# Kernel tuning notes

Measured on AMD Instinct MI355X. Metric: run time of the kernel, lower is better.

Reference implementation:

```python
import jax, jax.numpy as jnp
import numpy as np

D_MODEL = 1024
N_HEADS = 16
HEAD_DIM = D_MODEL // N_HEADS  # 64
WINDOW = 15
NUM_RANDOM = 2
B, L = 2, 2048


def setup_inputs() -> dict:
    key = jax.random.key(0)
    ks = jax.random.split(key, 5)
    x = jax.random.normal(ks[0], (B, L, D_MODEL), dtype=jnp.float32)
    # rotary angles: theta[t, j] = t / 10000^(2j/head_dim), shape [1, L, head_dim//2]
    inv_freq = 1.0 / (10000.0 ** (jnp.arange(0, HEAD_DIM, 2, dtype=jnp.float32) / HEAD_DIM))
    t = jnp.arange(L, dtype=jnp.float32)
    freqs = (t[:, None] * inv_freq[None, :])[None].astype(jnp.float32)  # [1,L,32]
    scale = 0.02
    wq = jax.random.normal(ks[1], (D_MODEL, D_MODEL), dtype=jnp.float32) * scale
    wk = jax.random.normal(ks[2], (D_MODEL, D_MODEL), dtype=jnp.float32) * scale
    wv = jax.random.normal(ks[3], (D_MODEL, D_MODEL), dtype=jnp.float32) * scale
    wo = jax.random.normal(ks[4], (D_MODEL, D_MODEL), dtype=jnp.float32) * scale
    return {"x": x, "freqs": freqs, "wq": wq, "wk": wk, "wv": wv, "wo": wo}


def _rope(t, cos, sin):
    # t: [B,H,L,hd]; interpret last dim as (hd/2, 2) complex pairs and rotate.
    tr = t.reshape(*t.shape[:-1], -1, 2)
    re, im = tr[..., 0], tr[..., 1]
    out_re = re * cos - im * sin
    out_im = re * sin + im * cos
    return jnp.stack([out_re, out_im], axis=-1).reshape(t.shape)


def _bigbird_mask(Lq):
    ii = jnp.arange(Lq)[:, None]
    jj = jnp.arange(Lq)[None, :]
    causal = jj <= ii
    window = jnp.abs(ii - jj) <= (WINDOW // 2)
    glob = (ii == 0) | (jj == 0)
    # random mask: per row i, NUM_RANDOM indices uniform in [0, i]
    rkey = jax.random.key(42)
    u = jax.random.uniform(rkey, (Lq, NUM_RANDOM))
    ridx = jnp.floor(u * (jnp.arange(Lq, dtype=jnp.float32)[:, None] + 1.0)).astype(jnp.int32)
    rmask = jnp.zeros((Lq, Lq), dtype=bool).at[jnp.arange(Lq)[:, None], ridx].set(True)
    # rows with <= NUM_RANDOM causal options attend to all of them
    rmask = rmask | (causal & (ii < NUM_RANDOM))
    return (causal & (window | rmask)) | glob  # [L,L]


def reference(x, freqs, wq, wk, wv, wo):
    b, l, _ = x.shape
    q = (x @ wq.T).reshape(b, l, N_HEADS, HEAD_DIM).transpose(0, 2, 1, 3)  # [B,H,L,hd]
    k = (x @ wk.T).reshape(b, l, N_HEADS, HEAD_DIM).transpose(0, 2, 1, 3)
    v = (x @ wv.T).reshape(b, l, N_HEADS, HEAD_DIM).transpose(0, 2, 1, 3)
    cos = jnp.cos(freqs[:, :l])[:, None]  # [1,1,L,hd/2]
    sin = jnp.sin(freqs[:, :l])[:, None]
    q = _rope(q, cos, sin)
    k = _rope(k, cos, sin)
    attn_mask = _bigbird_mask(l)  # [L,L], broadcast over B,H
    scale = 1.0 / jnp.sqrt(jnp.float32(HEAD_DIM))
    scores = jnp.einsum("bhqd,bhkd->bhqk", q, k) * scale
    scores = jnp.where(attn_mask[None, None], scores, jnp.finfo(scores.dtype).min)
    p = jax.nn.softmax(scores, axis=-1)
    out = jnp.einsum("bhqk,bhkd->bhqd", p, v)
    out = out.transpose(0, 2, 1, 3).reshape(b, l, D_MODEL)
    return out @ wo.T
```

## Files before the change

kernel.cpp:

```cpp
#include <hip/hip_runtime.h>
#include <math.h>

#define SEQ_L 2048
#define DM 1024
#define NH 16
#define HD 64
#define NB 2
#define KD 1024
#define ND 1024

typedef __bf16 bf16;
typedef __bf16 bf16x8 __attribute__((ext_vector_type(8)));
typedef __bf16 bf16x4 __attribute__((ext_vector_type(4)));
typedef __bf16 bf16x2 __attribute__((ext_vector_type(2)));
typedef float f32x4 __attribute__((ext_vector_type(4)));

__device__ inline uint32_t rotl32(uint32_t v, int n) { return (v << n) | (v >> (32 - n)); }

__device__ inline void threefry(uint32_t x0, uint32_t x1, uint32_t* o0, uint32_t* o1) {
  const uint32_t ks0 = 0u, ks1 = 42u, ks2 = 0u ^ 42u ^ 0x1BD11BDAu;
  x0 += ks0; x1 += ks1;
#define TF_R(rr) { x0 += x1; x1 = rotl32(x1, rr); x1 ^= x0; }
  TF_R(13) TF_R(15) TF_R(26) TF_R(6)
  x0 += ks1; x1 += ks2 + 1u;
  TF_R(17) TF_R(29) TF_R(16) TF_R(24)
  x0 += ks2; x1 += ks0 + 2u;
  TF_R(13) TF_R(15) TF_R(26) TF_R(6)
  x0 += ks0; x1 += ks1 + 3u;
  TF_R(17) TF_R(29) TF_R(16) TF_R(24)
  x0 += ks1; x1 += ks2 + 4u;
  TF_R(13) TF_R(15) TF_R(26) TF_R(6)
  x0 += ks2; x1 += ks0 + 5u;
#undef TF_R
  *o0 = x0; *o1 = x1;
}

__device__ inline int rand_col(int i, int s) {
  uint32_t o0, o1;
  threefry(0u, (uint32_t)(2 * i + s), &o0, &o1);
  uint32_t bits = o0 ^ o1;
  float u = __uint_as_float((bits >> 9) | 0x3f800000u) - 1.0f;
  return (int)floorf(u * (float)(i + 1));
}

__global__ void prep_kernel(const float* __restrict__ x,
                            const float* __restrict__ w0, const float* __restrict__ w1,
                            const float* __restrict__ w2, const float* __restrict__ w3,
                            const float* __restrict__ freqs,
                            bf16* __restrict__ xb,
                            bf16* __restrict__ o0, bf16* __restrict__ o1,
                            bf16* __restrict__ o2, bf16* __restrict__ o3,
                            int* __restrict__ ctab, float2* __restrict__ rtab) {
  const int bx = blockIdx.x;
  const int t = threadIdx.x;
  if (bx < 8192) {
    const float* src;
    bf16* dst;
    int idx;
    if (bx < 4096) { src = x; dst = xb; idx = bx * 256 + t; }
    else {
      int widx = bx - 4096;
      int wsel = widx >> 10;
      switch (wsel) {
        case 0: src = w0; dst = o0; break;
        case 1: src = w1; dst = o1; break;
        case 2: src = w2; dst = o2; break;
        default: src = w3; dst = o3; break;
      }
      idx = (widx & 1023) * 256 + t;
    }
    float4 vv = ((const float4*)src)[idx];
    bf16x4 ov;
    ov[0] = (bf16)vv.x; ov[1] = (bf16)vv.y; ov[2] = (bf16)vv.z; ov[3] = (bf16)vv.w;
    *(bf16x4*)(dst + (size_t)idx * 4) = ov;
    return;
  }
  if (bx < 8200) {
    const int i = (bx - 8192) * 256 + t;
    int cols[11]; int nc = 0;
    if (i >= 1) {
      int lo = i - 7; if (lo < 0) lo = 0;
      for (int j = lo; j <= i; ++j) cols[nc++] = j;
      if (lo > 0) cols[nc++] = 0;
#pragma unroll
      for (int s = 0; s < 2; ++s) {
        int rj = rand_col(i, s);
        bool dup = false;
        for (int c2 = 0; c2 < nc; ++c2) dup |= (cols[c2] == rj);
        if (!dup) cols[nc++] = rj;
      }
    }
    for (int c2 = nc; c2 < 11; ++c2) cols[c2] = -1;
#pragma unroll
    for (int c2 = 0; c2 < 11; ++c2) ctab[i * 12 + c2] = cols[c2];
    ctab[i * 12 + 11] = nc;
    return;
  }
  const int idx = (bx - 8200) * 256 + t;
  float s, c;
  sincosf(freqs[idx], &s, &c);
  rtab[idx] = make_float2(c, s);
}

__device__ inline void gld16(const bf16* g, bf16* l) {
  __builtin_amdgcn_global_load_lds((const __attribute__((address_space(1))) void*)g,
                                   (__attribute__((address_space(3))) void*)l, 16, 0, 0);
}

__global__ __launch_bounds__(256, 4) void qkv_gemm_kernel(
    const bf16* __restrict__ xb, const bf16* __restrict__ wqb, const bf16* __restrict__ wkb,
    const bf16* __restrict__ wvb, bf16* __restrict__ qb, bf16* __restrict__ kb, bf16* __restrict__ vb,
    const float2* __restrict__ rtab) {
  __shared__ __align__(16) bf16 As[64 * 64];
  __shared__ __align__(16) bf16 Bs[3][64 * 64];
  const bf16* Ws[3] = {wqb, wkb, wvb};
  bf16* Ds[3] = {qb, kb, vb};

  const int t = threadIdx.x;
  const int lane = t & 63;
  const int w = t >> 6;
  const int wm = (w >> 1) * 32;
  const int wn = (w & 1) * 32;
  const int m0 = blockIdx.x * 64;
  const int n0 = blockIdx.y * 64;
  const int l15 = lane & 15;
  const int kq = lane >> 4;

  f32x4 acc[3][2][2] = {};

  for (int k0 = 0; k0 < KD; k0 += 64) {
#pragma unroll
    for (int n = 0; n < 2; ++n) {
      const int s = n * 256 + t;
      const int row = s >> 3;
      const int ch = (s & 7) ^ (row & 7);
      gld16(xb + (size_t)(m0 + row) * KD + k0 + ch * 8, As + s * 8);
    }
#pragma unroll
    for (int j = 0; j < 3; ++j)
#pragma unroll
      for (int n = 0; n < 2; ++n) {
        const int s = n * 256 + t;
        const int row = s >> 3;
        const int ch = (s & 7) ^ (row & 7);
        gld16(Ws[j] + (size_t)(n0 + row) * KD + k0 + ch * 8, &Bs[j][s * 8]);
      }
    __syncthreads();
#pragma unroll
    for (int ks = 0; ks < 2; ++ks) {
      const int cb = ks * 4 + kq;
      bf16x8 af[2];
#pragma unroll
      for (int mt = 0; mt < 2; ++mt) {
        const int row = wm + mt * 16 + l15;
        af[mt] = *(const bf16x8*)(As + row * 64 + ((cb ^ (row & 7)) * 8));
      }
#pragma unroll
      for (int j = 0; j < 3; ++j) {
        bf16x8 bfr[2];
#pragma unroll
        for (int nt = 0; nt < 2; ++nt) {
          const int row = wn + nt * 16 + l15;
          bfr[nt] = *(const bf16x8*)(&Bs[j][row * 64 + ((cb ^ (row & 7)) * 8)]);
        }
#pragma unroll
        for (int mt = 0; mt < 2; ++mt)
#pragma unroll
          for (int nt = 0; nt < 2; ++nt)
            acc[j][mt][nt] = __builtin_amdgcn_mfma_f32_16x16x32_bf16(af[mt], bfr[nt], acc[j][mt][nt], 0, 0, 0);
      }
    }
    __syncthreads();
  }
  const int colb = n0 + wn + l15;
  const int rowb = m0 + wm + (lane >> 4) * 4;
  const int odd = l15 & 1;
#pragma unroll
  for (int j = 0; j < 3; ++j) {
    bf16* D = Ds[j];
    const bool dorope = (j < 2);
#pragma unroll
    for (int mt = 0; mt < 2; ++mt)
#pragma unroll
      for (int nt = 0; nt < 2; ++nt) {
        const int col = colb + nt * 16;
        const int jj = (col & 63) >> 1;
#pragma unroll
        for (int rr = 0; rr < 4; ++rr) {
          float val = acc[j][mt][nt][rr];
          float other = __shfl_xor(val, 1);
          if (!odd) {
            const int row = rowb + mt * 16 + rr;
            float lo, hi;
            if (dorope) {
              float2 cs = rtab[(row & (SEQ_L - 1)) * 32 + jj];
              lo = val * cs.x - other * cs.y;
              hi = val * cs.y + other * cs.x;
            } else { lo = val; hi = other; }
            bf16x2 p; p[0] = (bf16)lo; p[1] = (bf16)hi;
            *(bf16x2*)(D + (size_t)row * ND + col) = p;
          }
        }
      }
  }
}

__global__ __launch_bounds__(256, 2) void out_gemm_kernel(
    bf16* __restrict__ ab, const bf16* __restrict__ wob, float* __restrict__ out,
    const float* __restrict__ pm, const float* __restrict__ pz, const float* __restrict__ pv) {
  const int t = threadIdx.x;
  const int m0 = blockIdx.x * 64;
  const int n0 = blockIdx.y * 128;

  if (blockIdx.x == 0 || blockIdx.x == 32) {
    const int b = blockIdx.x == 0 ? 0 : 1;
#pragma unroll
    for (int e = t; e < DM; e += 256) {
      const int h = e >> 6, d = e & 63;
      const int base = b * 128 + h * 8;
      float M = -1e30f;
#pragma unroll
      for (int c = 0; c < 8; ++c) M = fmaxf(M, pm[base + c]);
      float Z = 0.f, od = 0.f;
#pragma unroll
      for (int c = 0; c < 8; ++c) {
        float sc = __expf(pm[base + c] - M);
        Z += pz[base + c] * sc;
        od += pv[(base + c) * 64 + d] * sc;
      }
      ab[(size_t)b * SEQ_L * DM + e] = (bf16)(od / Z);
    }
    __syncthreads();
  }

  __shared__ __align__(16) bf16 As[64 * 64];
  __shared__ __align__(16) bf16 Bs[128 * 64];
  const int lane = t & 63;
  const int wave = t >> 6;
  const int wm = (wave >> 1) * 32;
  const int wn = (wave & 1) * 64;
  const int l15 = lane & 15;
  const int kq = lane >> 4;

  f32x4 acc[2][4] = {};

  for (int k0 = 0; k0 < KD; k0 += 64) {
#pragma unroll
    for (int n = 0; n < 2; ++n) {
      const int s = n * 256 + t;
      const int row = s >> 3;
      const int ch = (s & 7) ^ (row & 7);
      gld16(ab + (size_t)(m0 + row) * KD + k0 + ch * 8, As + s * 8);
    }
#pragma unroll
    for (int n = 0; n < 4; ++n) {
      const int s = n * 256 + t;
      const int row = s >> 3;
      const int ch = (s & 7) ^ (row & 7);
      gld16(wob + (size_t)(n0 + row) * KD + k0 + ch * 8, Bs + s * 8);
    }
    __syncthreads();
#pragma unroll
    for (int ks = 0; ks < 2; ++ks) {
      const int cb = ks * 4 + kq;
      bf16x8 af[2], bfr[4];
#pragma unroll
      for (int mt = 0; mt < 2; ++mt) {
        const int row = wm + mt * 16 + l15;
        af[mt] = *(const bf16x8*)(As + row * 64 + ((cb ^ (row & 7)) * 8));
      }
#pragma unroll
      for (int nt = 0; nt < 4; ++nt) {
        const int row = wn + nt * 16 + l15;
        bfr[nt] = *(const bf16x8*)(Bs + row * 64 + ((cb ^ (row & 7)) * 8));
      }
#pragma unroll
      for (int mt = 0; mt < 2; ++mt)
#pragma unroll
        for (int nt = 0; nt < 4; ++nt)
          acc[mt][nt] = __builtin_amdgcn_mfma_f32_16x16x32_bf16(af[mt], bfr[nt], acc[mt][nt], 0, 0, 0);
    }
    __syncthreads();
  }
  const int colb = n0 + wn + l15;
  const int rowb = m0 + wm + (lane >> 4) * 4;
#pragma unroll
  for (int mt = 0; mt < 2; ++mt)
#pragma unroll
    for (int nt = 0; nt < 4; ++nt)
#pragma unroll
      for (int rr = 0; rr < 4; ++rr)
        out[(size_t)(rowb + mt * 16 + rr) * ND + colb + nt * 16] = acc[mt][nt][rr];
}

__global__ __launch_bounds__(256, 2) void attn_kernel(const bf16* __restrict__ q, const bf16* __restrict__ k,
                                                      const bf16* __restrict__ v, bf16* __restrict__ o,
                                                      const int* __restrict__ ctab,
                                                      float* __restrict__ pm, float* __restrict__ pz,
                                                      float* __restrict__ pv) {
  const int t = threadIdx.x;
  const int lane = t & 63;
  const int w = t >> 6;

  __shared__ float sbuf[256];
  __shared__ float redm[4], redz[4];
  __shared__ float part[4][64];

  if (blockIdx.x >= 256) {
    const int sbx = blockIdx.x - 256;
    const int b = sbx >> 9;
    const int tt = sbx & 511;
    const int tile = ((tt & 7) << 6) + (tt >> 3);
    const int i = tile * 4 + 1 + w;
    if (i >= SEQ_L) return;
    const size_t bb = (size_t)b * SEQ_L * DM;
    const int eo = lane * 16;

    const bf16* qrow = q + bb + (size_t)i * DM + eo;
    bf16x8 qv0 = *(const bf16x8*)(qrow);
    bf16x8 qv1 = *(const bf16x8*)(qrow + 8);

    const int4* cp = (const int4*)(ctab + i * 12);
    int4 ca = cp[0], cb = cp[1], cc = cp[2];
    int cols[11] = {ca.x, ca.y, ca.z, ca.w, cb.x, cb.y, cb.z, cb.w, cc.x, cc.y, cc.z};

    bf16x8 kv[11][2], vv[11][2];
#pragma unroll
    for (int c = 0; c < 11; ++c) {
      int cj = cols[c] < 0 ? 0 : cols[c];
      const bf16* krow = k + bb + (size_t)cj * DM + eo;
      kv[c][0] = *(const bf16x8*)(krow);
      kv[c][1] = *(const bf16x8*)(krow + 8);
    }
#pragma unroll
    for (int c = 0; c < 11; ++c) {
      int cj = cols[c] < 0 ? 0 : cols[c];
      const bf16* vrow = v + bb + (size_t)cj * DM + eo;
      vv[c][0] = *(const bf16x8*)(vrow);
      vv[c][1] = *(const bf16x8*)(vrow + 8);
    }

    float sv[11];
#pragma unroll
    for (int c = 0; c < 11; ++c) {
      float acc = 0.f;
#pragma unroll
      for (int e = 0; e < 8; ++e)
        acc += (float)qv0[e] * (float)kv[c][0][e] + (float)qv1[e] * (float)kv[c][1][e];
      sv[c] = acc;
    }
#pragma unroll
    for (int c = 0; c < 11; ++c) {
      sv[c] += __shfl_xor(sv[c], 1);
      sv[c] += __shfl_xor(sv[c], 2);
      sv[c] = cols[c] < 0 ? -1e30f : sv[c] * 0.125f;
    }
    float m = -1e30f;
#pragma unroll
    for (int c = 0; c < 11; ++c) m = fmaxf(m, sv[c]);
    float z = 0.f;
#pragma unroll
    for (int c = 0; c < 11; ++c) { sv[c] = __expf(sv[c] - m); z += sv[c]; }
    const float inv = 1.f / z;

    float oa[16] = {};
#pragma unroll
    for (int c = 0; c < 11; ++c) {
#pragma unroll
      for (int e = 0; e < 8; ++e) {
        oa[e]     += sv[c] * (float)vv[c][0][e];
        oa[8 + e] += sv[c] * (float)vv[c][1][e];
      }
    }
    bf16x8 ov0, ov1;
#pragma unroll
    for (int e = 0; e < 8; ++e) {
      ov0[e] = (bf16)(oa[e] * inv);
      ov1[e] = (bf16)(oa[8 + e] * inv);
    }
    bf16* orow = o + bb + (size_t)i * DM + eo;
    *(bf16x8*)(orow) = ov0;
    *(bf16x8*)(orow + 8) = ov1;
    return;
  }

  const int idx = blockIdx.x;
  const int b = idx >> 7;
  const int rem = idx & 127;
  const int h = rem >> 3;
  const int c = rem & 7;
  const size_t hb = (size_t)b * SEQ_L * DM + (size_t)h * HD;
  const int j = c * 256 + t;

  bf16x8 qv8[8];
#pragma unroll
  for (int cc = 0; cc < 8; ++cc) qv8[cc] = *(const bf16x8*)(q + hb + cc * 8);

  float acc = 0.f;
#pragma unroll
  for (int cc = 0; cc < 8; ++cc) {
    bf16x8 kv = *(const bf16x8*)(k + hb + (size_t)j * DM + cc * 8);
#pragma unroll
    for (int e = 0; e < 8; ++e) acc += (float)qv8[cc][e] * (float)kv[e];
  }
  float s = acc * 0.125f;
  float mloc = s;
#pragma unroll
  for (int off = 32; off > 0; off >>= 1) mloc = fmaxf(mloc, __shfl_xor(mloc, off));
  if (lane == 0) redm[w] = mloc;
  __syncthreads();
  const float m = fmaxf(fmaxf(redm[0], redm[1]), fmaxf(redm[2], redm[3]));

  float e = __expf(s - m);
  sbuf[t] = e;
  float zloc = e;
#pragma unroll
  for (int off = 32; off > 0; off >>= 1) zloc += __shfl_xor(zloc, off);
  if (lane == 0) redz[w] = zloc;
  __syncthreads();
  const float zc = redz[0] + redz[1] + redz[2] + redz[3];

  float oa = 0.f;
  for (int jj = w; jj < 256; jj += 4)
    oa += sbuf[jj] * (float)v[hb + (size_t)(c * 256 + jj) * DM + lane];
  part[w][lane] = oa;
  __syncthreads();
  if (t < 64) pv[idx * 64 + t] = part[0][t] + part[1][t] + part[2][t] + part[3][t];
  if (t == 0) { pm[idx] = m; pz[idx] = zc; }
}

extern "C" void kernel_launch(void* const* d_in, const int* in_sizes, int n_in,
                              void* d_out, int out_size, void* d_ws, size_t ws_size,
                              hipStream_t stream) {
  const float* x     = (const float*)d_in[0];
  const float* freqs = (const float*)d_in[1];
  const float* wq    = (const float*)d_in[2];
  const float* wk    = (const float*)d_in[3];
  const float* wv    = (const float*)d_in[4];
  const float* wo    = (const float*)d_in[5];
  float* out = (float*)d_out;

  char* ws = (char*)d_ws;
  bf16* xb  = (bf16*)(ws + 0);
  bf16* wqb = (bf16*)(ws + 8388608);
  bf16* wkb = (bf16*)(ws + 10485760);
  bf16* wvb = (bf16*)(ws + 12582912);
  bf16* wob = (bf16*)(ws + 14680064);
  bf16* qb  = (bf16*)(ws + 16777216);
  bf16* kb  = (bf16*)(ws + 25165824);
  bf16* vb  = (bf16*)(ws + 33554432);
  bf16* ab  = (bf16*)(ws + 41943040);
  int*    ctab = (int*)(ws + 50331648);
  float*  pm   = (float*)(ws + 50462720);
  float*  pz   = (float*)(ws + 50463744);
  float*  pv   = (float*)(ws + 50464768);
  float2* rtab = (float2*)(ws + 50593792);
  (void)ws_size;

  prep_kernel<<<8456, 256, 0, stream>>>(x, wq, wk, wv, wo, freqs, xb, wqb, wkb, wvb, wob, ctab, rtab);
  qkv_gemm_kernel<<<dim3(64, 16), 256, 0, stream>>>(xb, wqb, wkb, wvb, qb, kb, vb, rtab);
  attn_kernel<<<dim3(1280, 1), 256, 0, stream>>>(qb, kb, vb, ab, ctab, pm, pz, pv);
  out_gemm_kernel<<<dim3(64, 8), 256, 0, stream>>>(ab, wob, out, pm, pz, pv);
}
```

Before: 162.9 us.

## Double-buffer LDS tiles in QKV and output GEMMs with K-step of 32

```diff
diff --git a/kernel.cpp b/kernel.cpp
--- a/kernel.cpp
+++ b/kernel.cpp
@@ -111,8 +111,8 @@
     const bf16* __restrict__ xb, const bf16* __restrict__ wqb, const bf16* __restrict__ wkb,
     const bf16* __restrict__ wvb, bf16* __restrict__ qb, bf16* __restrict__ kb, bf16* __restrict__ vb,
     const float2* __restrict__ rtab) {
-  __shared__ __align__(16) bf16 As[64 * 64];
-  __shared__ __align__(16) bf16 Bs[3][64 * 64];
+  __shared__ __align__(16) bf16 As[2][64 * 32];
+  __shared__ __align__(16) bf16 Bs[2][3][64 * 32];
   const bf16* Ws[3] = {wqb, wkb, wvb};
   bf16* Ds[3] = {qb, kb, vb};
 
@@ -126,51 +126,50 @@
   const int l15 = lane & 15;
   const int kq = lane >> 4;
 
+  const int srow = t >> 2;
+  const int sch = (t & 3) ^ ((srow >> 1) & 3);
+  const size_t soff = (size_t)srow * KD + sch * 8;
+  const bf16* gA = xb + (size_t)m0 * KD + soff;
+  const bf16* gB[3];
+#pragma unroll
+  for (int j = 0; j < 3; ++j) gB[j] = Ws[j] + (size_t)n0 * KD + soff;
+
   f32x4 acc[3][2][2] = {};
 
-  for (int k0 = 0; k0 < KD; k0 += 64) {
-#pragma unroll
-    for (int n = 0; n < 2; ++n) {
-      const int s = n * 256 + t;
-      const int row = s >> 3;
-      const int ch = (s & 7) ^ (row & 7);
-      gld16(xb + (size_t)(m0 + row) * KD + k0 + ch * 8, As + s * 8);
-    }
-#pragma unroll
-    for (int j = 0; j < 3; ++j)
-#pragma unroll
-      for (int n = 0; n < 2; ++n) {
-        const int s = n * 256 + t;
-        const int row = s >> 3;
-        const int ch = (s & 7) ^ (row & 7);
-        gld16(Ws[j] + (size_t)(n0 + row) * KD + k0 + ch * 8, &Bs[j][s * 8]);
-      }
+  gld16(gA, &As[0][t * 8]);
+#pragma unroll
+  for (int j = 0; j < 3; ++j) gld16(gB[j], &Bs[0][j][t * 8]);
+  __syncthreads();
+
+  int p = 0;
+  for (int k0 = 0; k0 < KD; k0 += 32) {
+    if (k0 + 32 < KD) {
+      gld16(gA + k0 + 32, &As[p ^ 1][t * 8]);
+#pragma unroll
+      for (int j = 0; j < 3; ++j) gld16(gB[j] + k0 + 32, &Bs[p ^ 1][j][t * 8]);
+    }
+    bf16x8 af[2];
+#pragma unroll
+    for (int mt = 0; mt < 2; ++mt) {
+      const int row = wm + mt * 16 + l15;
+      af[mt] = *(const bf16x8*)(&As[p][row * 32 + ((kq ^ ((row >> 1) & 3)) * 8)]);
+    }
+#pragma unroll
+    for (int j = 0; j < 3; ++j) {
+      bf16x8 bfr[2];
+#pragma unroll
+      for (int nt = 0; nt < 2; ++nt) {
+        const int row = wn + nt * 16 + l15;
+        bfr[nt] = *(const bf16x8*)(&Bs[p][j][row * 32 + ((kq ^ ((row >> 1) & 3)) * 8)]);
+      }
+#pragma unroll
+      for (int mt = 0; mt < 2; ++mt)
+#pragma unroll
+        for (int nt = 0; nt < 2; ++nt)
+          acc[j][mt][nt] = __builtin_amdgcn_mfma_f32_16x16x32_bf16(af[mt], bfr[nt], acc[j][mt][nt], 0, 0, 0);
+    }
     __syncthreads();
-#pragma unroll
-    for (int ks = 0; ks < 2; ++ks) {
-      const int cb = ks * 4 + kq;
-      bf16x8 af[2];
-#pragma unroll
-      for (int mt = 0; mt < 2; ++mt) {
-        const int row = wm + mt * 16 + l15;
-        af[mt] = *(const bf16x8*)(As + row * 64 + ((cb ^ (row & 7)) * 8));
-      }
-#pragma unroll
-      for (int j = 0; j < 3; ++j) {
-        bf16x8 bfr[2];
-#pragma unroll
-        for (int nt = 0; nt < 2; ++nt) {
-          const int row = wn + nt * 16 + l15;
-          bfr[nt] = *(const bf16x8*)(&Bs[j][row * 64 + ((cb ^ (row & 7)) * 8)]);
-        }
-#pragma unroll
-        for (int mt = 0; mt < 2; ++mt)
-#pragma unroll
-          for (int nt = 0; nt < 2; ++nt)
-            acc[j][mt][nt] = __builtin_amdgcn_mfma_f32_16x16x32_bf16(af[mt], bfr[nt], acc[j][mt][nt], 0, 0, 0);
-      }
-    }
-    __syncthreads();
+    p ^= 1;
   }
   const int colb = n0 + wn + l15;
   const int rowb = m0 + wm + (lane >> 4) * 4;
@@ -197,8 +196,8 @@
               lo = val * cs.x - other * cs.y;
               hi = val * cs.y + other * cs.x;
             } else { lo = val; hi = other; }
-            bf16x2 p; p[0] = (bf16)lo; p[1] = (bf16)hi;
-            *(bf16x2*)(D + (size_t)row * ND + col) = p;
+            bf16x2 p2; p2[0] = (bf16)lo; p2[1] = (bf16)hi;
+            *(bf16x2*)(D + (size_t)row * ND + col) = p2;
           }
         }
       }
@@ -233,8 +232,8 @@
     __syncthreads();
   }
 
-  __shared__ __align__(16) bf16 As[64 * 64];
-  __shared__ __align__(16) bf16 Bs[128 * 64];
+  __shared__ __align__(16) bf16 As[2][64 * 32];
+  __shared__ __align__(16) bf16 Bs[2][128 * 32];
   const int lane = t & 63;
   const int wave = t >> 6;
   const int wm = (wave >> 1) * 32;
@@ -244,43 +243,50 @@
 
   f32x4 acc[2][4] = {};
 
-  for (int k0 = 0; k0 < KD; k0 += 64) {
-#pragma unroll
-    for (int n = 0; n < 2; ++n) {
-      const int s = n * 256 + t;
-      const int row = s >> 3;
-      const int ch = (s & 7) ^ (row & 7);
-      gld16(ab + (size_t)(m0 + row) * KD + k0 + ch * 8, As + s * 8);
-    }
-#pragma unroll
-    for (int n = 0; n < 4; ++n) {
-      const int s = n * 256 + t;
-      const int row = s >> 3;
-      const int ch = (s & 7) ^ (row & 7);
-      gld16(wob + (size_t)(n0 + row) * KD + k0 + ch * 8, Bs + s * 8);
-    }
+  const int srowA = t >> 2;
+  const int schA = (t & 3) ^ ((srowA >> 1) & 3);
+  const bf16* gA = ab + (size_t)(m0 + srowA) * KD + schA * 8;
+  const bf16* gB[2];
+  int sB[2];
+#pragma unroll
+  for (int n = 0; n < 2; ++n) {
+    const int s = n * 256 + t;
+    const int row = s >> 2;
+    const int ch = (s & 3) ^ ((row >> 1) & 3);
+    gB[n] = wob + (size_t)(n0 + row) * KD + ch * 8;
+    sB[n] = s;
+  }
+
+  gld16(gA, &As[0][t * 8]);
+#pragma unroll
+  for (int n = 0; n < 2; ++n) gld16(gB[n], &Bs[0][sB[n] * 8]);
+  __syncthreads();
+
+  int p = 0;
+  for (int k0 = 0; k0 < KD; k0 += 32) {
+    if (k0 + 32 < KD) {
+      gld16(gA + k0 + 32, &As[p ^ 1][t * 8]);
+#pragma unroll
+      for (int n = 0; n < 2; ++n) gld16(gB[n] + k0 + 32, &Bs[p ^ 1][sB[n] * 8]);
+    }
+    bf16x8 af[2], bfr[4];
+#pragma unroll
+    for (int mt = 0; mt < 2; ++mt) {
+      const int row = wm + mt * 16 + l15;
+      af[mt] = *(const bf16x8*)(&As[p][row * 32 + ((kq ^ ((row >> 1) & 3)) * 8)]);
+    }
+#pragma unroll
+    for (int nt = 0; nt < 4; ++nt) {
+      const int row = wn + nt * 16 + l15;
+      bfr[nt] = *(const bf16x8*)(&Bs[p][row * 32 + ((kq ^ ((row >> 1) & 3)) * 8)]);
+    }
+#pragma unroll
+    for (int mt = 0; mt < 2; ++mt)
+#pragma unroll
+      for (int nt = 0; nt < 4; ++nt)
+        acc[mt][nt] = __builtin_amdgcn_mfma_f32_16x16x32_bf16(af[mt], bfr[nt], acc[mt][nt], 0, 0, 0);
     __syncthreads();
-#pragma unroll
-    for (int ks = 0; ks < 2; ++ks) {
-      const int cb = ks * 4 + kq;
-      bf16x8 af[2], bfr[4];
-#pragma unroll
-      for (int mt = 0; mt < 2; ++mt) {
-        const int row = wm + mt * 16 + l15;
-        af[mt] = *(const bf16x8*)(As + row * 64 + ((cb ^ (row & 7)) * 8));
-      }
-#pragma unroll
-      for (int nt = 0; nt < 4; ++nt) {
-        const int row = wn + nt * 16 + l15;
-        bfr[nt] = *(const bf16x8*)(Bs + row * 64 + ((cb ^ (row & 7)) * 8));
-      }
-#pragma unroll
-      for (int mt = 0; mt < 2; ++mt)
-#pragma unroll
-        for (int nt = 0; nt < 4; ++nt)
-          acc[mt][nt] = __builtin_amdgcn_mfma_f32_16x16x32_bf16(af[mt], bfr[nt], acc[mt][nt], 0, 0, 0);
-    }
-    __syncthreads();
+    p ^= 1;
   }
   const int colb = n0 + wn + l15;
   const int rowb = m0 + wm + (lane >> 4) * 4;
```

Result: slower. 174.4 us (+7.1%).

## Rewrite QKV GEMM as 256x256 tiled, double-buffered 512-thread kernel over fused weights

Applied to the files above, without the earlier changes.

```diff
diff --git a/kernel.cpp b/kernel.cpp
--- a/kernel.cpp
+++ b/kernel.cpp
@@ -107,102 +107,169 @@
                                    (__attribute__((address_space(3))) void*)l, 16, 0, 0);
 }
 
-__global__ __launch_bounds__(256, 4) void qkv_gemm_kernel(
-    const bf16* __restrict__ xb, const bf16* __restrict__ wqb, const bf16* __restrict__ wkb,
-    const bf16* __restrict__ wvb, bf16* __restrict__ qb, bf16* __restrict__ kb, bf16* __restrict__ vb,
+#define BAR() do { asm volatile("" ::: "memory"); __builtin_amdgcn_s_barrier(); asm volatile("" ::: "memory"); } while (0)
+
+template <int VM, bool DOSTAGE>
+__device__ __forceinline__ void qkv_ktile(
+    const bf16* curA, const bf16* curB, bf16* nxtA, bf16* nxtB,
+    const bf16* pA, const bf16* pB, int stageK, int t8,
+    int aOff, int bOff, int c0, int c1, f32x4 (&acc)[8][4]) {
+  bf16x8 af[4], bv[4];
+
+  if constexpr (DOSTAGE) {
+    gld16(pA + stageK, nxtA + t8);
+    gld16(pA + 65536 + stageK, nxtA + 4096 + t8);
+  }
+  asm volatile("s_waitcnt vmcnt(%0)" :: "n"(VM) : "memory");
+  BAR();
+#pragma unroll
+  for (int i = 0; i < 4; ++i) af[i] = *(const bf16x8*)(curA + aOff + i * 1024 + c0);
+#pragma unroll
+  for (int n = 0; n < 4; ++n) bv[n] = *(const bf16x8*)(curB + bOff + n * 1024 + c0);
+  __builtin_amdgcn_s_setprio(1);
+#pragma unroll
+  for (int i = 0; i < 4; ++i)
+#pragma unroll
+    for (int n = 0; n < 4; ++n)
+      acc[i][n] = __builtin_amdgcn_mfma_f32_16x16x32_bf16(af[i], bv[n], acc[i][n], 0, 0, 0);
+  __builtin_amdgcn_s_setprio(0);
+  BAR();
+
+#pragma unroll
+  for (int i = 0; i < 4; ++i) af[i] = *(const bf16x8*)(curA + aOff + (4 + i) * 1024 + c0);
+  if constexpr (DOSTAGE) {
+    gld16(pA + 131072 + stageK, nxtA + 8192 + t8);
+    gld16(pA + 196608 + stageK, nxtA + 12288 + t8);
+  }
+  BAR();
+  __builtin_amdgcn_s_setprio(1);
+#pragma unroll
+  for (int i = 0; i < 4; ++i)
+#pragma unroll
+    for (int n = 0; n < 4; ++n)
+      acc[4 + i][n] = __builtin_amdgcn_mfma_f32_16x16x32_bf16(af[i], bv[n], acc[4 + i][n], 0, 0, 0);
+  __builtin_amdgcn_s_setprio(0);
+  BAR();
+
+#pragma unroll
+  for (int i = 0; i < 4; ++i) af[i] = *(const bf16x8*)(curA + aOff + i * 1024 + c1);
+#pragma unroll
+  for (int n = 0; n < 4; ++n) bv[n] = *(const bf16x8*)(curB + bOff + n * 1024 + c1);
+  if constexpr (DOSTAGE) {
+    gld16(pB + stageK, nxtB + t8);
+    gld16(pB + 65536 + stageK, nxtB + 4096 + t8);
+  }
+  BAR();
+  __builtin_amdgcn_s_setprio(1);
+#pragma unroll
+  for (int i = 0; i < 4; ++i)
+#pragma unroll
+    for (int n = 0; n < 4; ++n)
+      acc[i][n] = __builtin_amdgcn_mfma_f32_16x16x32_bf16(af[i], bv[n], acc[i][n], 0, 0, 0);
+  __builtin_amdgcn_s_setprio(0);
+  BAR();
+
+#pragma unroll
+  for (int i = 0; i < 4; ++i) af[i] = *(const bf16x8*)(curA + aOff + (4 + i) * 1024 + c1);
+  if constexpr (DOSTAGE) {
+    gld16(pB + 131072 + stageK, nxtB + 8192 + t8);
+    gld16(pB + 196608 + stageK, nxtB + 12288 + t8);
+  }
+  BAR();
+  __builtin_amdgcn_s_setprio(1);
+#pragma unroll
+  for (int i = 0; i < 4; ++i)
+#pragma unroll
+    for (int n = 0; n < 4; ++n)
+      acc[4 + i][n] = __builtin_amdgcn_mfma_f32_16x16x32_bf16(af[i], bv[n], acc[4 + i][n], 0, 0, 0);
+  __builtin_amdgcn_s_setprio(0);
+  BAR();
+}
+
+__global__ __launch_bounds__(512, 2) void qkv_gemm_kernel(
+    const bf16* __restrict__ xb, const bf16* __restrict__ wqkv,
+    bf16* __restrict__ qb, bf16* __restrict__ kb, bf16* __restrict__ vb,
     const float2* __restrict__ rtab) {
-  __shared__ __align__(16) bf16 As[64 * 64];
-  __shared__ __align__(16) bf16 Bs[3][64 * 64];
-  const bf16* Ws[3] = {wqb, wkb, wvb};
-  bf16* Ds[3] = {qb, kb, vb};
+  __shared__ __align__(16) bf16 Al[2][256 * 64];
+  __shared__ __align__(16) bf16 Bl[2][256 * 64];
 
   const int t = threadIdx.x;
   const int lane = t & 63;
-  const int w = t >> 6;
-  const int wm = (w >> 1) * 32;
-  const int wn = (w & 1) * 32;
-  const int m0 = blockIdx.x * 64;
-  const int n0 = blockIdx.y * 64;
   const int l15 = lane & 15;
   const int kq = lane >> 4;
-
-  f32x4 acc[3][2][2] = {};
-
-  for (int k0 = 0; k0 < KD; k0 += 64) {
-#pragma unroll
-    for (int n = 0; n < 2; ++n) {
-      const int s = n * 256 + t;
-      const int row = s >> 3;
-      const int ch = (s & 7) ^ (row & 7);
-      gld16(xb + (size_t)(m0 + row) * KD + k0 + ch * 8, As + s * 8);
-    }
-#pragma unroll
-    for (int j = 0; j < 3; ++j)
-#pragma unroll
-      for (int n = 0; n < 2; ++n) {
-        const int s = n * 256 + t;
-        const int row = s >> 3;
-        const int ch = (s & 7) ^ (row & 7);
-        gld16(Ws[j] + (size_t)(n0 + row) * KD + k0 + ch * 8, &Bs[j][s * 8]);
-      }
-    __syncthreads();
-#pragma unroll
-    for (int ks = 0; ks < 2; ++ks) {
-      const int cb = ks * 4 + kq;
-      bf16x8 af[2];
-#pragma unroll
-      for (int mt = 0; mt < 2; ++mt) {
-        const int row = wm + mt * 16 + l15;
-        af[mt] = *(const bf16x8*)(As + row * 64 + ((cb ^ (row & 7)) * 8));
-      }
-#pragma unroll
-      for (int j = 0; j < 3; ++j) {
-        bf16x8 bfr[2];
-#pragma unroll
-        for (int nt = 0; nt < 2; ++nt) {
-          const int row = wn + nt * 16 + l15;
-          bfr[nt] = *(const bf16x8*)(&Bs[j][row * 64 + ((cb ^ (row & 7)) * 8)]);
+  const int w = t >> 6;
+  const int wm = w >> 2;
+  const int wn = w & 3;
+
+  int id = blockIdx.x;
+  id = (id & 7) * 24 + (id >> 3);
+  const int bx = id / 12;
+  const int by = id % 12;
+  const int m0 = bx * 256;
+  const int n0g = by * 256;
+
+  const int r0 = t >> 3;
+  const int kg0 = (t & 7) ^ (r0 & 7);
+  const bf16* pA = xb + (size_t)(m0 + r0) * KD + kg0 * 8;
+  const bf16* pB = wqkv + (size_t)(n0g + r0) * KD + kg0 * 8;
+  const int t8 = t * 8;
+
+  const int aOff = (wm * 128 + l15) * 64;
+  const int bOff = (wn * 64 + l15) * 64;
+  const int swz = l15 & 7;
+  const int c0 = (kq ^ swz) * 8;
+  const int c1 = ((4 + kq) ^ swz) * 8;
+
+  f32x4 acc[8][4] = {};
+
+  bf16* A0 = &Al[0][0]; bf16* A1 = &Al[1][0];
+  bf16* B0 = &Bl[0][0]; bf16* B1 = &Bl[1][0];
+
+  gld16(pA, A0 + t8);
+  gld16(pA + 65536, A0 + 4096 + t8);
+  gld16(pA + 131072, A0 + 8192 + t8);
+  gld16(pA + 196608, A0 + 12288 + t8);
+  gld16(pB, B0 + t8);
+  gld16(pB + 65536, B0 + 4096 + t8);
+  gld16(pB + 131072, B0 + 8192 + t8);
+  gld16(pB + 196608, B0 + 12288 + t8);
+
+  for (int kt = 0; kt < 14; kt += 2) {
+    qkv_ktile<2, true>(A0, B0, A1, B1, pA, pB, (kt + 1) * 64, t8, aOff, bOff, c0, c1, acc);
+    qkv_ktile<2, true>(A1, B1, A0, B0, pA, pB, (kt + 2) * 64, t8, aOff, bOff, c0, c1, acc);
+  }
+  qkv_ktile<2, true>(A0, B0, A1, B1, pA, pB, 15 * 64, t8, aOff, bOff, c0, c1, acc);
+  qkv_ktile<0, false>(A1, B1, A0, B0, pA, pB, 0, t8, aOff, bOff, c0, c1, acc);
+
+  const int j = by >> 2;
+  bf16* D = (j == 0) ? qb : (j == 1 ? kb : vb);
+  const bool dorope = (j < 2);
+  const int colb = (by & 3) * 256 + wn * 64 + l15;
+  const int rowb = m0 + wm * 128 + (lane >> 4) * 4;
+  const int odd = l15 & 1;
+#pragma unroll
+  for (int mf = 0; mf < 8; ++mf)
+#pragma unroll
+    for (int nf = 0; nf < 4; ++nf) {
+      const int col = colb + nf * 16;
+      const int jj = (col & 63) >> 1;
+#pragma unroll
+      for (int rr = 0; rr < 4; ++rr) {
+        float val = acc[mf][nf][rr];
+        float other = __shfl_xor(val, 1);
+        if (!odd) {
+          const int row = rowb + mf * 16 + rr;
+          float lo, hi;
+          if (dorope) {
+            float2 cs = rtab[(row & (SEQ_L - 1)) * 32 + jj];
+            lo = val * cs.x - other * cs.y;
+            hi = val * cs.y + other * cs.x;
+          } else { lo = val; hi = other; }
+          bf16x2 p2; p2[0] = (bf16)lo; p2[1] = (bf16)hi;
+          *(bf16x2*)(D + (size_t)row * ND + col) = p2;
         }
-#pragma unroll
-        for (int mt = 0; mt < 2; ++mt)
-#pragma unroll
-          for (int nt = 0; nt < 2; ++nt)
-            acc[j][mt][nt] = __builtin_amdgcn_mfma_f32_16x16x32_bf16(af[mt], bfr[nt], acc[j][mt][nt], 0, 0, 0);
-      }
-    }
-    __syncthreads();
-  }
-  const int colb = n0 + wn + l15;
-  const int rowb = m0 + wm + (lane >> 4) * 4;
-  const int odd = l15 & 1;
-#pragma unroll
-  for (int j = 0; j < 3; ++j) {
-    bf16* D = Ds[j];
-    const bool dorope = (j < 2);
-#pragma unroll
-    for (int mt = 0; mt < 2; ++mt)
-#pragma unroll
-      for (int nt = 0; nt < 2; ++nt) {
-        const int col = colb + nt * 16;
-        const int jj = (col & 63) >> 1;
-#pragma unroll
-        for (int rr = 0; rr < 4; ++rr) {
-          float val = acc[j][mt][nt][rr];
-          float other = __shfl_xor(val, 1);
-          if (!odd) {
-            const int row = rowb + mt * 16 + rr;
-            float lo, hi;
-            if (dorope) {
-              float2 cs = rtab[(row & (SEQ_L - 1)) * 32 + jj];
-              lo = val * cs.x - other * cs.y;
-              hi = val * cs.y + other * cs.x;
-            } else { lo = val; hi = other; }
-            bf16x2 p; p[0] = (bf16)lo; p[1] = (bf16)hi;
-            *(bf16x2*)(D + (size_t)row * ND + col) = p;
-          }
-        }
-      }
-  }
+      }
+    }
 }
 
 __global__ __launch_bounds__(256, 2) void out_gemm_kernel(
@@ -458,7 +525,7 @@
   (void)ws_size;
 
   prep_kernel<<<8456, 256, 0, stream>>>(x, wq, wk, wv, wo, freqs, xb, wqb, wkb, wvb, wob, ctab, rtab);
-  qkv_gemm_kernel<<<dim3(64, 16), 256, 0, stream>>>(xb, wqb, wkb, wvb, qb, kb, vb, rtab);
+  qkv_gemm_kernel<<<dim3(192), 512, 0, stream>>>(xb, wqb, qb, kb, vb, rtab);
   attn_kernel<<<dim3(1280, 1), 256, 0, stream>>>(qb, kb, vb, ab, ctab, pm, pz, pv);
   out_gemm_kernel<<<dim3(64, 8), 256, 0, stream>>>(ab, wob, out, pm, pz, pv);
 }
```

Result: slower. 187.4 us (+15.0%).

## Retile QKV GEMM to 128x128 tiles over fused QKV weight with XCD-aware block remap

Applied to the files above, without the earlier changes.

```diff
diff --git a/kernel.cpp b/kernel.cpp
--- a/kernel.cpp
+++ b/kernel.cpp
@@ -107,102 +107,98 @@
                                    (__attribute__((address_space(3))) void*)l, 16, 0, 0);
 }
 
-__global__ __launch_bounds__(256, 4) void qkv_gemm_kernel(
-    const bf16* __restrict__ xb, const bf16* __restrict__ wqb, const bf16* __restrict__ wkb,
-    const bf16* __restrict__ wvb, bf16* __restrict__ qb, bf16* __restrict__ kb, bf16* __restrict__ vb,
+__global__ __launch_bounds__(256, 3) void qkv_gemm_kernel(
+    const bf16* __restrict__ xb, const bf16* __restrict__ wqkv,
+    bf16* __restrict__ qb, bf16* __restrict__ kb, bf16* __restrict__ vb,
     const float2* __restrict__ rtab) {
-  __shared__ __align__(16) bf16 As[64 * 64];
-  __shared__ __align__(16) bf16 Bs[3][64 * 64];
-  const bf16* Ws[3] = {wqb, wkb, wvb};
-  bf16* Ds[3] = {qb, kb, vb};
+  __shared__ __align__(16) bf16 As[128 * 64];
+  __shared__ __align__(16) bf16 Bs[128 * 64];
 
   const int t = threadIdx.x;
   const int lane = t & 63;
   const int w = t >> 6;
-  const int wm = (w >> 1) * 32;
-  const int wn = (w & 1) * 32;
-  const int m0 = blockIdx.x * 64;
-  const int n0 = blockIdx.y * 64;
+  const int wm = (w >> 1) * 64;
+  const int wn = (w & 1) * 64;
   const int l15 = lane & 15;
   const int kq = lane >> 4;
 
-  f32x4 acc[3][2][2] = {};
+  int id = blockIdx.x;
+  id = (id & 7) * 96 + (id >> 3);
+  const int bx = id / 24;
+  const int by = id % 24;
+  const int m0 = bx * 128;
+  const int n0g = by * 128;
+
+  f32x4 acc[4][4] = {};
 
   for (int k0 = 0; k0 < KD; k0 += 64) {
 #pragma unroll
-    for (int n = 0; n < 2; ++n) {
+    for (int n = 0; n < 4; ++n) {
       const int s = n * 256 + t;
       const int row = s >> 3;
       const int ch = (s & 7) ^ (row & 7);
       gld16(xb + (size_t)(m0 + row) * KD + k0 + ch * 8, As + s * 8);
     }
 #pragma unroll
-    for (int j = 0; j < 3; ++j)
-#pragma unroll
-      for (int n = 0; n < 2; ++n) {
-        const int s = n * 256 + t;
-        const int row = s >> 3;
-        const int ch = (s & 7) ^ (row & 7);
-        gld16(Ws[j] + (size_t)(n0 + row) * KD + k0 + ch * 8, &Bs[j][s * 8]);
-      }
+    for (int n = 0; n < 4; ++n) {
+      const int s = n * 256 + t;
+      const int row = s >> 3;
+      const int ch = (s & 7) ^ (row & 7);
+      gld16(wqkv + (size_t)(n0g + row) * KD + k0 + ch * 8, Bs + s * 8);
+    }
     __syncthreads();
 #pragma unroll
     for (int ks = 0; ks < 2; ++ks) {
       const int cb = ks * 4 + kq;
-      bf16x8 af[2];
-#pragma unroll
-      for (int mt = 0; mt < 2; ++mt) {
+      bf16x8 af[4], bv[4];
+#pragma unroll
+      for (int mt = 0; mt < 4; ++mt) {
         const int row = wm + mt * 16 + l15;
         af[mt] = *(const bf16x8*)(As + row * 64 + ((cb ^ (row & 7)) * 8));
       }
 #pragma unroll
-      for (int j = 0; j < 3; ++j) {
-        bf16x8 bfr[2];
-#pragma unroll
-        for (int nt = 0; nt < 2; ++nt) {
-          const int row = wn + nt * 16 + l15;
-          bfr[nt] = *(const bf16x8*)(&Bs[j][row * 64 + ((cb ^ (row & 7)) * 8)]);
-        }
-#pragma unroll
-        for (int mt = 0; mt < 2; ++mt)
-#pragma unroll
-          for (int nt = 0; nt < 2; ++nt)
-            acc[j][mt][nt] = __builtin_amdgcn_mfma_f32_16x16x32_bf16(af[mt], bfr[nt], acc[j][mt][nt], 0, 0, 0);
-      }
+      for (int nt = 0; nt < 4; ++nt) {
+        const int row = wn + nt * 16 + l15;
+        bv[nt] = *(const bf16x8*)(Bs + row * 64 + ((cb ^ (row & 7)) * 8));
+      }
+#pragma unroll
+      for (int mt = 0; mt < 4; ++mt)
+#pragma unroll
+        for (int nt = 0; nt < 4; ++nt)
+          acc[mt][nt] = __builtin_amdgcn_mfma_f32_16x16x32_bf16(af[mt], bv[nt], acc[mt][nt], 0, 0, 0);
     }
     __syncthreads();
   }
-  const int colb = n0 + wn + l15;
+
+  const int j = by >> 3;
+  bf16* D = (j == 0) ? qb : (j == 1 ? kb : vb);
+  const bool dorope = (j < 2);
+  const int colb = (by & 7) * 128 + wn + l15;
   const int rowb = m0 + wm + (lane >> 4) * 4;
   const int odd = l15 & 1;
 #pragma unroll
-  for (int j = 0; j < 3; ++j) {
-    bf16* D = Ds[j];
-    const bool dorope = (j < 2);
-#pragma unroll
-    for (int mt = 0; mt < 2; ++mt)
-#pragma unroll
-      for (int nt = 0; nt < 2; ++nt) {
-        const int col = colb + nt * 16;
-        const int jj = (col & 63) >> 1;
-#pragma unroll
-        for (int rr = 0; rr < 4; ++rr) {
-          float val = acc[j][mt][nt][rr];
-          float other = __shfl_xor(val, 1);
-          if (!odd) {
-            const int row = rowb + mt * 16 + rr;
-            float lo, hi;
-            if (dorope) {
-              float2 cs = rtab[(row & (SEQ_L - 1)) * 32 + jj];
-              lo = val * cs.x - other * cs.y;
-              hi = val * cs.y + other * cs.x;
-            } else { lo = val; hi = other; }
-            bf16x2 p; p[0] = (bf16)lo; p[1] = (bf16)hi;
-            *(bf16x2*)(D + (size_t)row * ND + col) = p;
-          }
+  for (int mf = 0; mf < 4; ++mf)
+#pragma unroll
+    for (int nf = 0; nf < 4; ++nf) {
+      const int col = colb + nf * 16;
+      const int jj = (col & 63) >> 1;
+#pragma unroll
+      for (int rr = 0; rr < 4; ++rr) {
+        float val = acc[mf][nf][rr];
+        float other = __shfl_xor(val, 1);
+        if (!odd) {
+          const int row = rowb + mf * 16 + rr;
+          float lo, hi;
+          if (dorope) {
+            float2 cs = rtab[(row & (SEQ_L - 1)) * 32 + jj];
+            lo = val * cs.x - other * cs.y;
+            hi = val * cs.y + other * cs.x;
+          } else { lo = val; hi = other; }
+          bf16x2 p2; p2[0] = (bf16)lo; p2[1] = (bf16)hi;
+          *(bf16x2*)(D + (size_t)row * ND + col) = p2;
         }
       }
-  }
+    }
 }
 
 __global__ __launch_bounds__(256, 2) void out_gemm_kernel(
@@ -458,7 +454,7 @@
   (void)ws_size;
 
   prep_kernel<<<8456, 256, 0, stream>>>(x, wq, wk, wv, wo, freqs, xb, wqb, wkb, wvb, wob, ctab, rtab);
-  qkv_gemm_kernel<<<dim3(64, 16), 256, 0, stream>>>(xb, wqb, wkb, wvb, qb, kb, vb, rtab);
+  qkv_gemm_kernel<<<dim3(768), 256, 0, stream>>>(xb, wqb, qb, kb, vb, rtab);
   attn_kernel<<<dim3(1280, 1), 256, 0, stream>>>(qb, kb, vb, ab, ctab, pm, pz, pv);
   out_gemm_kernel<<<dim3(64, 8), 256, 0, stream>>>(ab, wob, out, pm, pz, pv);
 }
```

Measured after the change: 165.1 us. About the same (+1.3%).
